# Kernel optimization log

Measured on AMD Instinct MI355X. Metric: run time of the kernel, lower is better.

## Reference

```python
import jax, jax.numpy as jnp
import numpy as np

K = 20
EPS = 1e-5  # BatchNorm eps; eval mode with running_mean=0, running_var=1


def _lrelu(x):
    return jnp.where(x >= 0, x, 0.2 * x)


def _bn(x, g, b):
    # eval-mode BN (fresh running stats: mean=0, var=1); channel axis = 1
    shape = (1, -1) + (1,) * (x.ndim - 2)
    return x * (g / jnp.sqrt(1.0 + EPS)).reshape(shape) + b.reshape(shape)


def _knn_idx(x, k):
    # x: (B, C, N). Negative squared euclidean distance, top-k = nearest.
    xx = jnp.sum(x * x, axis=1)                      # (B, N)
    inner = jnp.einsum('bcn,bcm->bnm', x, x)         # (B, N, N)
    neg_d = 2.0 * inner - xx[:, :, None] - xx[:, None, :]
    return jax.lax.top_k(neg_d, k)[1]                # (B, N, K)


def _gather(x, idx):
    # x: (B, C, N), idx: (B, N, K) -> (B, C, N, K)
    return jax.vmap(lambda xb, ib: xb[:, ib])(x, idx)


def setup_inputs() -> dict:
    key = jax.random.key(0)
    ks = jax.random.split(key, 32)
    B, N = 8, 2048
    d = {}
    d['x'] = jax.random.normal(ks[0], (B, 3, N), jnp.float32)

    def w(k_, o, i):
        return jax.random.normal(k_, (o, i), jnp.float32) * (1.0 / np.sqrt(i))

    d['W1'] = w(ks[1], 64, 3)
    d['W2'] = w(ks[2], 64, 64)
    d['W3'] = w(ks[3], 128, 64)
    d['W4'] = w(ks[4], 256, 128)
    d['W5'] = w(ks[5], 1024, 512)
    bn_dims = [64, 64, 128, 256, 1024, 512, 256]
    for i, c in enumerate(bn_dims):
        d[f'g{i+1}'] = 1.0 + 0.1 * jax.random.normal(ks[6 + 2 * i], (c,), jnp.float32)
        d[f'b{i+1}'] = 0.1 * jax.random.normal(ks[7 + 2 * i], (c,), jnp.float32)
    d['L1W'] = w(ks[20], 512, 2048)
    d['L2W'] = w(ks[21], 256, 512)
    d['L2b'] = 0.1 * jax.random.normal(ks[22], (256,), jnp.float32)
    d['L3W'] = w(ks[23], 40, 256)
    d['L3b'] = 0.1 * jax.random.normal(ks[24], (40,), jnp.float32)
    return d


def reference(x, W1, W2, W3, W4, W5,
              g1, b1, g2, b2, g3, b3, g4, b4, g5, b5, g6, b6, g7, b7,
              L1W, L2W, L2b, L3W, L3b):
    idx = _knn_idx(x, K)  # shared neighbor indices for all EdgeConv blocks

    h = _lrelu(_bn(jnp.einsum('oc,bcnk->bonk', W1, _gather(x, idx)), g1, b1))
    x1 = h.max(axis=-1)                               # (B, 64, N)
    h = _lrelu(_bn(jnp.einsum('oc,bcnk->bonk', W2, _gather(x1, idx)), g2, b2))
    x2 = h.max(axis=-1)                               # (B, 64, N)
    h = _lrelu(_bn(jnp.einsum('oc,bcnk->bonk', W3, _gather(x2, idx)), g3, b3))
    x3 = h.max(axis=-1)                               # (B, 128, N)
    h = _lrelu(_bn(jnp.einsum('oc,bcnk->bonk', W4, _gather(x3, idx)), g4, b4))
    x4 = h.max(axis=-1)                               # (B, 256, N)

    cat = jnp.concatenate([x1, x2, x3, x4], axis=1)   # (B, 512, N)
    h = _lrelu(_bn(jnp.einsum('oc,bcn->bon', W5, cat), g5, b5))  # (B, 1024, N)

    f = jnp.concatenate([h.max(axis=-1), h.mean(axis=-1)], axis=1)  # (B, 2048)
    f = _lrelu(_bn(f @ L1W.T, g6, b6))
    f = _lrelu(_bn(f @ L2W.T + L2b, g7, b7))          # dropout is identity in eval
    return f @ L3W.T + L3b                            # (B, 40)
```

## Files before the change

### kernel.cpp

```cpp
#include <hip/hip_runtime.h>
#include <math.h>


#define WS_IDX      0
#define WS_Y16      1310720
#define WS_XCAT16   9699328
#define WS_W16      26476544
#define WS_FMAX     27615232
#define WS_FSUM     27648000
#define WS_A1       27680768
#define WS_A2       27697152

typedef _Float16 f16x8 __attribute__((ext_vector_type(8)));
typedef float f32x4 __attribute__((ext_vector_type(4)));

struct F3 { float x, y, z; };

__device__ __forceinline__ float lrelu(float v) { return (v >= 0.f) ? v : 0.2f * v; }
__device__ __forceinline__ unsigned sortable_f32(float f) {
  unsigned b = __float_as_uint(f);
  return b ^ (((unsigned)((int)b >> 31)) | 0x80000000u);
}
__device__ __forceinline__ float desort_f32(unsigned u) {
  unsigned b = (u & 0x80000000u) ? (u ^ 0x80000000u) : ~u;
  return __uint_as_float(b);
}

__global__ __launch_bounds__(256) void knn_prep_kernel(
    const float* __restrict__ x, const float* __restrict__ W1,
    const float* __restrict__ g1, const float* __restrict__ b1,
    const float* __restrict__ W2, const float* __restrict__ W3,
    const float* __restrict__ W4, const float* __restrict__ W5,
    _Float16* __restrict__ w16, unsigned* __restrict__ fzero,
    int* __restrict__ idxo, _Float16* __restrict__ xcat) {
  __shared__ F3 pts_s[2048];
  __shared__ unsigned long long cand_s[8][60];
  __shared__ unsigned cnt_s[8];
  __shared__ int sel_s[8][20];
  int tid = threadIdx.x;

  if (blockIdx.x >= 2048) {
    int bid = blockIdx.x - 2048;
#pragma unroll
    for (int t = 0; t < 8; ++t) {
      int i = bid * 2048 + t * 256 + tid;
      if (i < 4096) w16[i] = (_Float16)W2[i];
      else if (i < 12288) w16[i] = (_Float16)W3[i - 4096];
      else if (i < 45056) w16[i] = (_Float16)W4[i - 12288];
      else if (i < 569344) w16[i] = (_Float16)W5[i - 45056];
      else fzero[i - 569344] = 0u;
    }
    return;
  }

  int lwave = tid >> 6, lane = tid & 63;
  int qbase = blockIdx.x * 8;
  int b = qbase >> 11;
  int nbase = qbase & 2047;
  const float* xb = x + b * 6144;
#pragma unroll
  for (int i = 0; i < 8; ++i) {
    int m = tid + i * 256;
    F3 p; p.x = xb[m]; p.y = xb[2048 + m]; p.z = xb[4096 + m];
    pts_s[m] = p;
  }
  if (lane == 0) cnt_s[lwave * 2] = 0, cnt_s[lwave * 2 + 1] = 0;
  __syncthreads();

  F3 q[2];
  float qw[2];
  unsigned lmax[2] = {0u, 0u};
#pragma unroll
  for (int qi = 0; qi < 2; ++qi) {
    q[qi] = pts_s[nbase + lwave * 2 + qi];
    qw[qi] = q[qi].x * q[qi].x + q[qi].y * q[qi].y + q[qi].z * q[qi].z;
  }
  for (int j = 0; j < 32; ++j) {
    F3 p = pts_s[j * 64 + lane];
    float pw = p.x * p.x + p.y * p.y + p.z * p.z;
#pragma unroll
    for (int qi = 0; qi < 2; ++qi) {
      float nd = 2.0f * (q[qi].x * p.x + q[qi].y * p.y + q[qi].z * p.z) -
                 qw[qi] - pw;
      unsigned key = sortable_f32(nd);
      lmax[qi] = (key > lmax[qi]) ? key : lmax[qi];
    }
  }
  unsigned lo[2] = {0u, 0u}, hi[2] = {0x8001u, 0x8001u};
  for (int it = 0; it < 16; ++it) {
#pragma unroll
    for (int qi = 0; qi < 2; ++qi) {
      unsigned mid = (lo[qi] + hi[qi] + 1) >> 1;
      int cnt = __popcll(__ballot(lmax[qi] >= (mid << 16)));
      if (cnt >= 20) lo[qi] = mid; else hi[qi] = mid;
    }
  }
  unsigned T[2] = {lo[0] << 16, lo[1] << 16};
  for (int j = 0; j < 32; ++j) {
    int m = j * 64 + lane;
    F3 p = pts_s[m];
    float pw = p.x * p.x + p.y * p.y + p.z * p.z;
#pragma unroll
    for (int qi = 0; qi < 2; ++qi) {
      float nd = 2.0f * (q[qi].x * p.x + q[qi].y * p.y + q[qi].z * p.z) -
                 qw[qi] - pw;
      unsigned key = sortable_f32(nd);
      if (key >= T[qi]) {
        unsigned pos = atomicAdd(&cnt_s[lwave * 2 + qi], 1u);
        if (pos < 60)
          cand_s[lwave * 2 + qi][pos] =
              (((unsigned long long)key) << 32) | (unsigned)(2047 - m);
      }
    }
  }
#pragma unroll
  for (int qi = 0; qi < 2; ++qi) {
    int qq = lwave * 2 + qi;
    int row = qbase + qq;
    int outb = row * 20;
    unsigned C = cnt_s[qq];
    if (C <= 60) {
      unsigned long long v = (lane < (int)C) ? ~cand_s[qq][lane] : ~0ull;
#pragma unroll
      for (int k = 2; k <= 64; k <<= 1) {
#pragma unroll
        for (int jj = k >> 1; jj > 0; jj >>= 1) {
          unsigned long long o = __shfl_xor(v, jj, 64);
          bool lower = (lane & jj) == 0;
          bool up = (lane & k) == 0;
          bool takeMin = (lower == up);
          bool sw = takeMin ? (o < v) : (o > v);
          v = sw ? o : v;
        }
      }
      if (lane < 20) {
        unsigned long long pack = ~v;
        int m = 2047 - (int)(pack & 0xFFFFFFFFu);
        idxo[outb + lane] = m;
        sel_s[qq][lane] = m;
      }
    } else {
      unsigned long long prev = ~0ull;
      for (int r = 0; r < 20; ++r) {
        unsigned long long best = 0ull;
        for (int j = 0; j < 32; ++j) {
          int m = j * 64 + lane;
          F3 p = pts_s[m];
          float pw = p.x * p.x + p.y * p.y + p.z * p.z;
          float nd = 2.0f * (q[qi].x * p.x + q[qi].y * p.y + q[qi].z * p.z) -
                     qw[qi] - pw;
          unsigned long long pk =
              (((unsigned long long)sortable_f32(nd)) << 32) |
              (unsigned)(2047 - m);
          bool ok = (pk < prev) & (pk > best);
          best = ok ? pk : best;
        }
#pragma unroll
        for (int off = 1; off < 64; off <<= 1) {
          unsigned long long o = __shfl_xor(best, off, 64);
          best = (o > best) ? o : best;
        }
        int m = 2047 - (int)(best & 0xFFFFFFFFu);
        if (lane == 0) { idxo[outb + r] = m; sel_s[qq][r] = m; }
        prev = best;
      }
    }
  }
  float w0 = W1[lane * 3 + 0], w1 = W1[lane * 3 + 1], w2 = W1[lane * 3 + 2];
  float inv = 1.0f / sqrtf(1.0f + 1e-5f);
  float sc = g1[lane] * inv, bi = b1[lane];
#pragma unroll
  for (int qi = 0; qi < 2; ++qi) {
    int qq = lwave * 2 + qi;
    int row = qbase + qq;
    float mx = -3.4e38f, mn = 3.4e38f;
#pragma unroll
    for (int k = 0; k < 20; ++k) {
      F3 p = pts_s[sel_s[qq][k]];
      float v = w0 * p.x + w1 * p.y + w2 * p.z;
      mx = fmaxf(mx, v);
      mn = fminf(mn, v);
    }
    float v = (sc >= 0.0f) ? mx : mn;
    xcat[row * 512 + lane] = (_Float16)lrelu(sc * v + bi);
  }
}

template <int C, int COFF>
__global__ __launch_bounds__(256) void gmax_kernel(const _Float16* __restrict__ y,
                                                   const int* __restrict__ idx,
                                                   const float* __restrict__ g,
                                                   const float* __restrict__ bb,
                                                   _Float16* __restrict__ xcat) {
  constexpr int TP = C / 8;
  int e = blockIdx.x * 256 + threadIdx.x;
  int c8 = e & (TP - 1);
  int pg = e / TP;
  int b = pg >> 11;
  const int* ix = idx + pg * 20;
  int mm[20];
#pragma unroll
  for (int k = 0; k < 20; ++k) mm[k] = ix[k];
  int base = b * 2048 * C + c8 * 8;
  float mx[8], mn[8];
#pragma unroll
  for (int i = 0; i < 8; ++i) { mx[i] = -3.4e38f; mn[i] = 3.4e38f; }
#pragma unroll
  for (int k = 0; k < 20; ++k) {
    f16x8 v = *(const f16x8*)&y[base + mm[k] * C];
#pragma unroll
    for (int i = 0; i < 8; ++i) {
      float f = (float)v[i];
      mx[i] = fmaxf(mx[i], f);
      mn[i] = fminf(mn[i], f);
    }
  }
  float inv = 1.0f / sqrtf(1.0f + 1e-5f);
  f16x8 outv;
#pragma unroll
  for (int i = 0; i < 8; ++i) {
    float s = g[c8 * 8 + i] * inv;
    float v = (s >= 0.0f) ? mx[i] : mn[i];
    outv[i] = (_Float16)lrelu(s * v + bb[c8 * 8 + i]);
  }
  *(f16x8*)&xcat[pg * 512 + COFF + c8 * 8] = outv;
}

template <int CIN, int COUT, int XOFF>
__global__ __launch_bounds__(256) void gemm_mfma(const _Float16* __restrict__ Wh,
                                                 const _Float16* __restrict__ Xc,
                                                 _Float16* __restrict__ Y) {
  constexpr int BN = (COUT < 128) ? COUT : 128;
  constexpr int MT = (BN == 128) ? 4 : 2;
  __shared__ _Float16 Xs[128 * 40];
  __shared__ _Float16 Ws[BN * 40];
  int tid = threadIdx.x;
  int lane = tid & 63, w = tid >> 6;
  int wm = (BN == 128) ? (w & 1) : w;
  int wn = (BN == 128) ? (w >> 1) : 0;
  int col = lane & 15, quad = lane >> 4;
  int pg0 = blockIdx.x * 128;
  int o0 = blockIdx.y * BN;
  int r0 = tid >> 2;
  int c8 = (tid & 3) * 8;
  f32x4 acc[MT][4] = {};
  for (int k0 = 0; k0 < CIN; k0 += 32) {
    f16x8 xa = *(const f16x8*)&Xc[(pg0 + r0) * 512 + XOFF + k0 + c8];
    f16x8 xb2 = *(const f16x8*)&Xc[(pg0 + r0 + 64) * 512 + XOFF + k0 + c8];
    f16x8 wa = *(const f16x8*)&Wh[(o0 + r0) * CIN + k0 + c8];
    f16x8 wb;
    if (BN == 128) wb = *(const f16x8*)&Wh[(o0 + r0 + 64) * CIN + k0 + c8];
    __syncthreads();
    *(f16x8*)&Xs[r0 * 40 + c8] = xa;
    *(f16x8*)&Xs[(r0 + 64) * 40 + c8] = xb2;
    *(f16x8*)&Ws[r0 * 40 + c8] = wa;
    if (BN == 128) *(f16x8*)&Ws[(r0 + 64) * 40 + c8] = wb;
    __syncthreads();
    f16x8 af[MT], bf[4];
#pragma unroll
    for (int t = 0; t < MT; ++t)
      af[t] = *(const f16x8*)&Xs[(wm * (MT * 16) + t * 16 + col) * 40 + quad * 8];
#pragma unroll
    for (int t = 0; t < 4; ++t)
      bf[t] = *(const f16x8*)&Ws[(wn * 64 + t * 16 + col) * 40 + quad * 8];
#pragma unroll
    for (int mt = 0; mt < MT; ++mt)
#pragma unroll
      for (int nt = 0; nt < 4; ++nt)
        acc[mt][nt] = __builtin_amdgcn_mfma_f32_16x16x32_f16(af[mt], bf[nt],
                                                             acc[mt][nt], 0, 0, 0);
  }
#pragma unroll
  for (int mt = 0; mt < MT; ++mt)
#pragma unroll
    for (int nt = 0; nt < 4; ++nt)
#pragma unroll
      for (int r = 0; r < 4; ++r) {
        int p = pg0 + wm * (MT * 16) + mt * 16 + quad * 4 + r;
        int ch = o0 + wn * 64 + nt * 16 + col;
        Y[p * COUT + ch] = (_Float16)acc[mt][nt][r];
      }
}

__global__ __launch_bounds__(256) void gemm5_kernel(
    const _Float16* __restrict__ Wh, const _Float16* __restrict__ Xc,
    const float* __restrict__ g5, const float* __restrict__ b5,
    unsigned* __restrict__ fmax, float* __restrict__ fsum) {
  __shared__ _Float16 Xs[128 * 40];
  __shared__ _Float16 Ws[128 * 40];
  __shared__ float pm[256], ps[256];
  int tid = threadIdx.x;
  int lane = tid & 63, w = tid >> 6;
  int wm = w & 1, wn = w >> 1;
  int col = lane & 15, quad = lane >> 4;
  int pg0 = blockIdx.x * 128;
  int o0 = blockIdx.y * 128;
  int r0 = tid >> 2;
  int c8 = (tid & 3) * 8;

  f32x4 acc[4][4] = {};
  for (int k0 = 0; k0 < 512; k0 += 32) {
    f16x8 xa = *(const f16x8*)&Xc[(pg0 + r0) * 512 + k0 + c8];
    f16x8 xb = *(const f16x8*)&Xc[(pg0 + r0 + 64) * 512 + k0 + c8];
    f16x8 wa = *(const f16x8*)&Wh[(o0 + r0) * 512 + k0 + c8];
    f16x8 wb = *(const f16x8*)&Wh[(o0 + r0 + 64) * 512 + k0 + c8];
    __syncthreads();
    *(f16x8*)&Xs[r0 * 40 + c8] = xa;
    *(f16x8*)&Xs[(r0 + 64) * 40 + c8] = xb;
    *(f16x8*)&Ws[r0 * 40 + c8] = wa;
    *(f16x8*)&Ws[(r0 + 64) * 40 + c8] = wb;
    __syncthreads();
    f16x8 af[4], bf[4];
#pragma unroll
    for (int t = 0; t < 4; ++t) {
      af[t] = *(const f16x8*)&Xs[(wm * 64 + t * 16 + col) * 40 + quad * 8];
      bf[t] = *(const f16x8*)&Ws[(wn * 64 + t * 16 + col) * 40 + quad * 8];
    }
#pragma unroll
    for (int mt = 0; mt < 4; ++mt)
#pragma unroll
      for (int nt = 0; nt < 4; ++nt)
        acc[mt][nt] = __builtin_amdgcn_mfma_f32_16x16x32_f16(af[mt], bf[nt],
                                                             acc[mt][nt], 0, 0, 0);
  }
  float inv = 1.0f / sqrtf(1.0f + 1e-5f);
#pragma unroll
  for (int nt = 0; nt < 4; ++nt) {
    int o = o0 + wn * 64 + nt * 16 + col;
    float sc = g5[o] * inv, bi = b5[o];
    float mx = -3.4e38f, sm = 0.f;
#pragma unroll
    for (int mt = 0; mt < 4; ++mt)
#pragma unroll
      for (int r = 0; r < 4; ++r) {
        float v = lrelu(acc[mt][nt][r] * sc + bi);
        mx = fmaxf(mx, v);
        sm += v;
      }
    mx = fmaxf(mx, __shfl_xor(mx, 16, 64));
    sm += __shfl_xor(sm, 16, 64);
    mx = fmaxf(mx, __shfl_xor(mx, 32, 64));
    sm += __shfl_xor(sm, 32, 64);
    if (quad == 0) {
      pm[wm * 128 + wn * 64 + nt * 16 + col] = mx;
      ps[wm * 128 + wn * 64 + nt * 16 + col] = sm;
    }
  }
  __syncthreads();
  if (tid < 128) {
    float m = fmaxf(pm[tid], pm[128 + tid]);
    float s = ps[tid] + ps[128 + tid];
    int b = pg0 >> 11;
    atomicMax(&fmax[b * 1024 + o0 + tid], sortable_f32(m));
    atomicAdd(&fsum[b * 1024 + o0 + tid], s);
  }
}

__global__ __launch_bounds__(256) void l1_kernel(const unsigned* __restrict__ fmax,
                                                 const float* __restrict__ fsum,
                                                 const float* __restrict__ L1W,
                                                 const float* __restrict__ g6,
                                                 const float* __restrict__ b6,
                                                 float* __restrict__ a1) {
  int gw = (blockIdx.x * 256 + threadIdx.x) >> 6;
  int lane = threadIdx.x & 63;
  int b = gw >> 9, o = gw & 511;
  float s = 0.f;
#pragma unroll
  for (int i = 0; i < 32; ++i) {
    int j = lane + i * 64;
    float fj = (j < 1024) ? desort_f32(fmax[b * 1024 + j])
                          : fsum[b * 1024 + j - 1024] * (1.0f / 2048.0f);
    s += fj * L1W[o * 2048 + j];
  }
#pragma unroll
  for (int off = 1; off < 64; off <<= 1) s += __shfl_xor(s, off, 64);
  if (lane == 0) {
    float scv = g6[o] / sqrtf(1.0f + 1e-5f);
    a1[b * 512 + o] = lrelu(s * scv + b6[o]);
  }
}

__global__ __launch_bounds__(256) void l2_kernel(const float* __restrict__ a1,
                                                 const float* __restrict__ L2W,
                                                 const float* __restrict__ L2b,
                                                 const float* __restrict__ g7,
                                                 const float* __restrict__ b7,
                                                 float* __restrict__ a2) {
  int gw = (blockIdx.x * 256 + threadIdx.x) >> 6;
  int lane = threadIdx.x & 63;
  int b = gw >> 8, o = gw & 255;
  float s = 0.f;
#pragma unroll
  for (int i = 0; i < 8; ++i) {
    int j = lane + i * 64;
    s += a1[b * 512 + j] * L2W[o * 512 + j];
  }
#pragma unroll
  for (int off = 1; off < 64; off <<= 1) s += __shfl_xor(s, off, 64);
  if (lane == 0) {
    float v = s + L2b[o];
    float scv = g7[o] / sqrtf(1.0f + 1e-5f);
    a2[b * 256 + o] = lrelu(v * scv + b7[o]);
  }
}

__global__ __launch_bounds__(256) void l3_kernel(const float* __restrict__ a2,
                                                 const float* __restrict__ L3W,
                                                 const float* __restrict__ L3b,
                                                 float* __restrict__ out) {
  int gw = (blockIdx.x * 256 + threadIdx.x) >> 6;
  int lane = threadIdx.x & 63;
  int b = gw / 40, o = gw % 40;
  float s = 0.f;
#pragma unroll
  for (int i = 0; i < 4; ++i) {
    int j = lane + i * 64;
    s += a2[b * 256 + j] * L3W[o * 256 + j];
  }
#pragma unroll
  for (int off = 1; off < 64; off <<= 1) s += __shfl_xor(s, off, 64);
  if (lane == 0) out[b * 40 + o] = s + L3b[o];
}

extern "C" void kernel_launch(void* const* d_in, const int* in_sizes, int n_in,
                              void* d_out, int out_size, void* d_ws, size_t ws_size,
                              hipStream_t stream) {
  const float* x = (const float*)d_in[0];
  const float* W1 = (const float*)d_in[1];
  const float* W2 = (const float*)d_in[2];
  const float* W3 = (const float*)d_in[3];
  const float* W4 = (const float*)d_in[4];
  const float* W5 = (const float*)d_in[5];
  const float* g1 = (const float*)d_in[6];  const float* b1 = (const float*)d_in[7];
  const float* g2 = (const float*)d_in[8];  const float* b2 = (const float*)d_in[9];
  const float* g3 = (const float*)d_in[10]; const float* b3 = (const float*)d_in[11];
  const float* g4 = (const float*)d_in[12]; const float* b4 = (const float*)d_in[13];
  const float* g5 = (const float*)d_in[14]; const float* b5 = (const float*)d_in[15];
  const float* g6 = (const float*)d_in[16]; const float* b6 = (const float*)d_in[17];
  const float* g7 = (const float*)d_in[18]; const float* b7 = (const float*)d_in[19];
  const float* L1W = (const float*)d_in[20];
  const float* L2W = (const float*)d_in[21];
  const float* L2b = (const float*)d_in[22];
  const float* L3W = (const float*)d_in[23];
  const float* L3b = (const float*)d_in[24];

  char* w = (char*)d_ws;
  int* idxb = (int*)(w + WS_IDX);
  _Float16* y16 = (_Float16*)(w + WS_Y16);
  _Float16* xcat16 = (_Float16*)(w + WS_XCAT16);
  _Float16* w16 = (_Float16*)(w + WS_W16);
  unsigned* fmax = (unsigned*)(w + WS_FMAX);
  float* fsum = (float*)(w + WS_FSUM);
  float* a1 = (float*)(w + WS_A1);
  float* a2 = (float*)(w + WS_A2);

  knn_prep_kernel<<<2334, 256, 0, stream>>>(x, W1, g1, b1, W2, W3, W4, W5,
                                            w16, fmax, idxb, xcat16);
  gemm_mfma<64, 64, 0><<<dim3(128, 1), 256, 0, stream>>>(w16, xcat16, y16);
  gmax_kernel<64, 64><<<512, 256, 0, stream>>>(y16, idxb, g2, b2, xcat16);
  gemm_mfma<64, 128, 64><<<dim3(128, 1), 256, 0, stream>>>(w16 + 4096, xcat16, y16);
  gmax_kernel<128, 128><<<1024, 256, 0, stream>>>(y16, idxb, g3, b3, xcat16);
  gemm_mfma<128, 256, 128><<<dim3(128, 2), 256, 0, stream>>>(w16 + 12288, xcat16, y16);
  gmax_kernel<256, 256><<<2048, 256, 0, stream>>>(y16, idxb, g4, b4, xcat16);
  gemm5_kernel<<<dim3(128, 8), 256, 0, stream>>>(w16 + 45056, xcat16, g5, b5, fmax, fsum);
  l1_kernel<<<1024, 256, 0, stream>>>(fmax, fsum, L1W, g6, b6, a1);
  l2_kernel<<<512, 256, 0, stream>>>(a1, L2W, L2b, g7, b7, a2);
  l3_kernel<<<80, 256, 0, stream>>>(a2, L3W, L3b, (float*)d_out);
}
```

Before: 236.9 us.

## Use direct global-to-LDS loads with XOR swizzle in GEMMs and fuse head layers

The MFMA GEMM kernels now stage tiles with global_load_lds 16-byte direct loads into unpadded LDS. A rotating column swizzle replaces the padding to avoid bank conflicts, removing the register round trip for staging. gemm5 reuses the tile LDS for its reduction scratch. The L2 and L3 linear kernels are fused into one 8-block kernel that keeps a2 in shared memory, saving a launch and a global round trip. This adds a tiny kernel with low parallelism, and a dead counter variable appears in the kNN kernel.

```diff
diff --git a/kernel.cpp b/kernel.cpp
--- a/kernel.cpp
+++ b/kernel.cpp
@@ -9,7 +9,6 @@
 #define WS_FMAX     27615232
 #define WS_FSUM     27648000
 #define WS_A1       27680768
-#define WS_A2       27697152
 
 typedef _Float16 f16x8 __attribute__((ext_vector_type(8)));
 typedef float f32x4 __attribute__((ext_vector_type(4)));
@@ -24,6 +23,11 @@
 __device__ __forceinline__ float desort_f32(unsigned u) {
   unsigned b = (u & 0x80000000u) ? (u ^ 0x80000000u) : ~u;
   return __uint_as_float(b);
+}
+__device__ __forceinline__ void gl_lds16(const _Float16* g, _Float16* l) {
+  __builtin_amdgcn_global_load_lds(
+      (const __attribute__((address_space(1))) void*)g,
+      (__attribute__((address_space(3))) void*)l, 16, 0, 0);
 }
 
 __global__ __launch_bounds__(256) void knn_prep_kernel(
@@ -96,6 +100,7 @@
     }
   }
   unsigned T[2] = {lo[0] << 16, lo[1] << 16};
+  int cnt[2] = {0, 0};
   for (int j = 0; j < 32; ++j) {
     int m = j * 64 + lane;
     F3 p = pts_s[m];
@@ -111,6 +116,7 @@
           cand_s[lwave * 2 + qi][pos] =
               (((unsigned long long)key) << 32) | (unsigned)(2047 - m);
       }
+      cnt[qi] = 0;
     }
   }
 #pragma unroll
@@ -232,8 +238,8 @@
                                                  _Float16* __restrict__ Y) {
   constexpr int BN = (COUT < 128) ? COUT : 128;
   constexpr int MT = (BN == 128) ? 4 : 2;
-  __shared__ _Float16 Xs[128 * 40];
-  __shared__ _Float16 Ws[BN * 40];
+  __shared__ _Float16 Xs[128 * 32];
+  __shared__ _Float16 Ws[BN * 32];
   int tid = threadIdx.x;
   int lane = tid & 63, w = tid >> 6;
   int wm = (BN == 128) ? (w & 1) : w;
@@ -242,27 +248,30 @@
   int pg0 = blockIdx.x * 128;
   int o0 = blockIdx.y * BN;
   int r0 = tid >> 2;
-  int c8 = (tid & 3) * 8;
+  int cg = ((tid & 3) + r0) & 3;
+  _Float16* xs_lo = Xs + w * 512;
+  _Float16* xs_hi = Xs + 64 * 32 + w * 512;
+  _Float16* ws_lo = Ws + w * 512;
+  _Float16* ws_hi = Ws + 64 * 32 + w * 512;
   f32x4 acc[MT][4] = {};
   for (int k0 = 0; k0 < CIN; k0 += 32) {
-    f16x8 xa = *(const f16x8*)&Xc[(pg0 + r0) * 512 + XOFF + k0 + c8];
-    f16x8 xb2 = *(const f16x8*)&Xc[(pg0 + r0 + 64) * 512 + XOFF + k0 + c8];
-    f16x8 wa = *(const f16x8*)&Wh[(o0 + r0) * CIN + k0 + c8];
-    f16x8 wb;
-    if (BN == 128) wb = *(const f16x8*)&Wh[(o0 + r0 + 64) * CIN + k0 + c8];
     __syncthreads();
-    *(f16x8*)&Xs[r0 * 40 + c8] = xa;
-    *(f16x8*)&Xs[(r0 + 64) * 40 + c8] = xb2;
-    *(f16x8*)&Ws[r0 * 40 + c8] = wa;
-    if (BN == 128) *(f16x8*)&Ws[(r0 + 64) * 40 + c8] = wb;
+    gl_lds16(&Xc[(pg0 + r0) * 512 + XOFF + k0 + cg * 8], xs_lo);
+    gl_lds16(&Xc[(pg0 + 64 + r0) * 512 + XOFF + k0 + cg * 8], xs_hi);
+    gl_lds16(&Wh[(o0 + r0) * CIN + k0 + cg * 8], ws_lo);
+    if (BN == 128) gl_lds16(&Wh[(o0 + 64 + r0) * CIN + k0 + cg * 8], ws_hi);
     __syncthreads();
     f16x8 af[MT], bf[4];
 #pragma unroll
-    for (int t = 0; t < MT; ++t)
-      af[t] = *(const f16x8*)&Xs[(wm * (MT * 16) + t * 16 + col) * 40 + quad * 8];
-#pragma unroll
-    for (int t = 0; t < 4; ++t)
-      bf[t] = *(const f16x8*)&Ws[(wn * 64 + t * 16 + col) * 40 + quad * 8];
+    for (int t = 0; t < MT; ++t) {
+      int R = wm * (MT * 16) + t * 16 + col;
+      af[t] = *(const f16x8*)&Xs[R * 32 + ((quad - R) & 3) * 8];
+    }
+#pragma unroll
+    for (int t = 0; t < 4; ++t) {
+      int R = wn * 64 + t * 16 + col;
+      bf[t] = *(const f16x8*)&Ws[R * 32 + ((quad - R) & 3) * 8];
+    }
 #pragma unroll
     for (int mt = 0; mt < MT; ++mt)
 #pragma unroll
@@ -286,9 +295,8 @@
     const _Float16* __restrict__ Wh, const _Float16* __restrict__ Xc,
     const float* __restrict__ g5, const float* __restrict__ b5,
     unsigned* __restrict__ fmax, float* __restrict__ fsum) {
-  __shared__ _Float16 Xs[128 * 40];
-  __shared__ _Float16 Ws[128 * 40];
-  __shared__ float pm[256], ps[256];
+  __shared__ _Float16 Xs[128 * 32];
+  __shared__ _Float16 Ws[128 * 32];
   int tid = threadIdx.x;
   int lane = tid & 63, w = tid >> 6;
   int wm = w & 1, wn = w >> 1;
@@ -296,25 +304,27 @@
   int pg0 = blockIdx.x * 128;
   int o0 = blockIdx.y * 128;
   int r0 = tid >> 2;
-  int c8 = (tid & 3) * 8;
+  int cg = ((tid & 3) + r0) & 3;
+  _Float16* xs_lo = Xs + w * 512;
+  _Float16* xs_hi = Xs + 64 * 32 + w * 512;
+  _Float16* ws_lo = Ws + w * 512;
+  _Float16* ws_hi = Ws + 64 * 32 + w * 512;
 
   f32x4 acc[4][4] = {};
   for (int k0 = 0; k0 < 512; k0 += 32) {
-    f16x8 xa = *(const f16x8*)&Xc[(pg0 + r0) * 512 + k0 + c8];
-    f16x8 xb = *(const f16x8*)&Xc[(pg0 + r0 + 64) * 512 + k0 + c8];
-    f16x8 wa = *(const f16x8*)&Wh[(o0 + r0) * 512 + k0 + c8];
-    f16x8 wb = *(const f16x8*)&Wh[(o0 + r0 + 64) * 512 + k0 + c8];
     __syncthreads();
-    *(f16x8*)&Xs[r0 * 40 + c8] = xa;
-    *(f16x8*)&Xs[(r0 + 64) * 40 + c8] = xb;
-    *(f16x8*)&Ws[r0 * 40 + c8] = wa;
-    *(f16x8*)&Ws[(r0 + 64) * 40 + c8] = wb;
+    gl_lds16(&Xc[(pg0 + r0) * 512 + k0 + cg * 8], xs_lo);
+    gl_lds16(&Xc[(pg0 + 64 + r0) * 512 + k0 + cg * 8], xs_hi);
+    gl_lds16(&Wh[(o0 + r0) * 512 + k0 + cg * 8], ws_lo);
+    gl_lds16(&Wh[(o0 + 64 + r0) * 512 + k0 + cg * 8], ws_hi);
     __syncthreads();
     f16x8 af[4], bf[4];
 #pragma unroll
     for (int t = 0; t < 4; ++t) {
-      af[t] = *(const f16x8*)&Xs[(wm * 64 + t * 16 + col) * 40 + quad * 8];
-      bf[t] = *(const f16x8*)&Ws[(wn * 64 + t * 16 + col) * 40 + quad * 8];
+      int Ra = wm * 64 + t * 16 + col;
+      int Rb = wn * 64 + t * 16 + col;
+      af[t] = *(const f16x8*)&Xs[Ra * 32 + ((quad - Ra) & 3) * 8];
+      bf[t] = *(const f16x8*)&Ws[Rb * 32 + ((quad - Rb) & 3) * 8];
     }
 #pragma unroll
     for (int mt = 0; mt < 4; ++mt)
@@ -323,7 +333,10 @@
         acc[mt][nt] = __builtin_amdgcn_mfma_f32_16x16x32_f16(af[mt], bf[nt],
                                                              acc[mt][nt], 0, 0, 0);
   }
+  float* pm = (float*)Xs;
+  float* ps = (float*)Ws;
   float inv = 1.0f / sqrtf(1.0f + 1e-5f);
+  __syncthreads();
 #pragma unroll
   for (int nt = 0; nt < 4; ++nt) {
     int o = o0 + wn * 64 + nt * 16 + col;
@@ -381,46 +394,51 @@
   }
 }
 
-__global__ __launch_bounds__(256) void l2_kernel(const float* __restrict__ a1,
-                                                 const float* __restrict__ L2W,
-                                                 const float* __restrict__ L2b,
-                                                 const float* __restrict__ g7,
-                                                 const float* __restrict__ b7,
-                                                 float* __restrict__ a2) {
-  int gw = (blockIdx.x * 256 + threadIdx.x) >> 6;
-  int lane = threadIdx.x & 63;
-  int b = gw >> 8, o = gw & 255;
-  float s = 0.f;
-#pragma unroll
-  for (int i = 0; i < 8; ++i) {
-    int j = lane + i * 64;
-    s += a1[b * 512 + j] * L2W[o * 512 + j];
-  }
-#pragma unroll
-  for (int off = 1; off < 64; off <<= 1) s += __shfl_xor(s, off, 64);
-  if (lane == 0) {
-    float v = s + L2b[o];
-    float scv = g7[o] / sqrtf(1.0f + 1e-5f);
-    a2[b * 256 + o] = lrelu(v * scv + b7[o]);
-  }
-}
-
-__global__ __launch_bounds__(256) void l3_kernel(const float* __restrict__ a2,
-                                                 const float* __restrict__ L3W,
-                                                 const float* __restrict__ L3b,
-                                                 float* __restrict__ out) {
-  int gw = (blockIdx.x * 256 + threadIdx.x) >> 6;
-  int lane = threadIdx.x & 63;
-  int b = gw / 40, o = gw % 40;
-  float s = 0.f;
-#pragma unroll
-  for (int i = 0; i < 4; ++i) {
-    int j = lane + i * 64;
-    s += a2[b * 256 + j] * L3W[o * 256 + j];
-  }
-#pragma unroll
-  for (int off = 1; off < 64; off <<= 1) s += __shfl_xor(s, off, 64);
-  if (lane == 0) out[b * 40 + o] = s + L3b[o];
+__global__ __launch_bounds__(256) void head23_kernel(
+    const float* __restrict__ a1, const float* __restrict__ L2W,
+    const float* __restrict__ L2b, const float* __restrict__ g7,
+    const float* __restrict__ b7, const float* __restrict__ L3W,
+    const float* __restrict__ L3b, float* __restrict__ out) {
+  __shared__ float a2s[256];
+  int b = blockIdx.x;
+  int tid = threadIdx.x, lane = tid & 63, w = tid >> 6;
+  const float* a1b = a1 + b * 512;
+  float inv = 1.0f / sqrtf(1.0f + 1e-5f);
+  for (int g8 = 0; g8 < 8; ++g8) {
+    int obase = w * 64 + g8 * 8;
+    float acc[8] = {};
+#pragma unroll
+    for (int i = 0; i < 8; ++i) {
+      int j = lane + i * 64;
+      float av = a1b[j];
+#pragma unroll
+      for (int oo = 0; oo < 8; ++oo) acc[oo] += av * L2W[(obase + oo) * 512 + j];
+    }
+#pragma unroll
+    for (int oo = 0; oo < 8; ++oo) {
+      float s = acc[oo];
+#pragma unroll
+      for (int off = 1; off < 64; off <<= 1) s += __shfl_xor(s, off, 64);
+      if (lane == 0) {
+        int o = obase + oo;
+        float v = s + L2b[o];
+        a2s[o] = lrelu(v * (g7[o] * inv) + b7[o]);
+      }
+    }
+  }
+  __syncthreads();
+  for (int t = 0; t < 10; ++t) {
+    int o = w + t * 4;
+    float s = 0.f;
+#pragma unroll
+    for (int i = 0; i < 4; ++i) {
+      int j = lane + i * 64;
+      s += a2s[j] * L3W[o * 256 + j];
+    }
+#pragma unroll
+    for (int off = 1; off < 64; off <<= 1) s += __shfl_xor(s, off, 64);
+    if (lane == 0) out[b * 40 + o] = s + L3b[o];
+  }
 }
 
 extern "C" void kernel_launch(void* const* d_in, const int* in_sizes, int n_in,
@@ -453,7 +471,6 @@
   unsigned* fmax = (unsigned*)(w + WS_FMAX);
   float* fsum = (float*)(w + WS_FSUM);
   float* a1 = (float*)(w + WS_A1);
-  float* a2 = (float*)(w + WS_A2);
 
   knn_prep_kernel<<<2334, 256, 0, stream>>>(x, W1, g1, b1, W2, W3, W4, W5,
                                             w16, fmax, idxb, xcat16);
@@ -465,6 +482,6 @@
   gmax_kernel<256, 256><<<2048, 256, 0, stream>>>(y16, idxb, g4, b4, xcat16);
   gemm5_kernel<<<dim3(128, 8), 256, 0, stream>>>(w16 + 45056, xcat16, g5, b5, fmax, fsum);
   l1_kernel<<<1024, 256, 0, stream>>>(fmax, fsum, L1W, g6, b6, a1);
-  l2_kernel<<<512, 256, 0, stream>>>(a1, L2W, L2b, g7, b7, a2);
-  l3_kernel<<<80, 256, 0, stream>>>(a2, L3W, L3b, (float*)d_out);
-}
+  head23_kernel<<<8, 256, 0, stream>>>(a1, L2W, L2b, g7, b7, L3W, L3b,
+                                       (float*)d_out);
+}
```

Measured after the change: 263.2 us. 1.11x slower.
